# Optimization experiments

Hardware: AMD Instinct MI355X
Metric: run time of the kernel (lower is better)

Reference implementation:

```python
import jax, jax.numpy as jnp
import numpy as np

D = 512       # d_model
H = 8         # n_heads
L = 6         # n_blocks
DFF = 2048    # d_ffn
IN_DIM = 4096
OUT_DIM = 1000
B = 8
S = 512
DK = D // H
EPS = 1e-5
NEG = -1e9    # masked_fill value from source (-1000000000.0)

# sinusoidal positional encoding table (matches Positional_Encoding)
_pos = np.arange(5000)[:, None].astype(np.float64)
_div = np.exp(np.arange(0, D, 2) * (-np.log(10000.0) / D))
_pe = np.zeros((5000, D), np.float32)
_pe[:, 0::2] = np.sin(_pos * _div)
_pe[:, 1::2] = np.cos(_pos * _div)
PE = jnp.asarray(_pe)


def _ln(x, g, b):
    m = jnp.mean(x, -1, keepdims=True)
    v = jnp.var(x, -1, keepdims=True)
    return (x - m) * jax.lax.rsqrt(v + EPS) * g + b


def _attn(q, k, v, causal):
    # q:[B,Sq,D], k/v:[B,Sk,D] -> multi-head attention with source's quirky mask
    b, sq, _ = q.shape
    sk = k.shape[1]
    q = q.reshape(b, sq, H, DK).transpose(0, 2, 1, 3)
    k = k.reshape(b, sk, H, DK).transpose(0, 2, 1, 3)
    v = v.reshape(b, sk, H, DK).transpose(0, 2, 1, 3)
    s = jnp.einsum('bhqd,bhkd->bhqk', q, k) / jnp.sqrt(jnp.asarray(DK, q.dtype))
    mask = s != 0.0  # faithful: source masks positions where score == padding (0)
    if causal:
        mask = mask & jnp.tril(jnp.ones((sq, sk), bool))
    s = jnp.where(mask, s, NEG)
    p = jax.nn.softmax(s, axis=-1)
    o = jnp.einsum('bhqk,bhkd->bhqd', p, v)
    return o.transpose(0, 2, 1, 3).reshape(b, sq, D)


def _ffn(x, w1, b1, w2, b2):
    return jax.nn.relu(x @ w1 + b1) @ w2 + b2


def setup_inputs() -> dict:
    key = jax.random.key(0)
    ks = iter(jax.random.split(key, 40))

    def w(shape, s=0.02):
        return jax.random.normal(next(ks), shape, jnp.float32) * s

    inp = {}
    inp['x'] = jax.random.randint(next(ks), (B, S), 0, IN_DIM)
    inp['target'] = jax.random.randint(next(ks), (B,), 0, OUT_DIM)
    inp['in_emb'] = w((IN_DIM, D), 1.0)
    inp['out_emb'] = w((OUT_DIM, D), 1.0)
    # encoder params (stacked over layers)
    inp['enc_qkv_w'] = w((L, 3, D, D))
    inp['enc_qkv_b'] = w((L, 3, D))
    inp['enc_ln1_g'] = jnp.ones((L, D), jnp.float32)
    inp['enc_ln1_b'] = jnp.zeros((L, D), jnp.float32)
    inp['enc_ffn1_w'] = w((L, D, DFF))
    inp['enc_ffn1_b'] = w((L, DFF))
    inp['enc_ffn2_w'] = w((L, DFF, D))
    inp['enc_ffn2_b'] = w((L, D))
    inp['enc_ln2_g'] = jnp.ones((L, D), jnp.float32)
    inp['enc_ln2_b'] = jnp.zeros((L, D), jnp.float32)
    # decoder params
    inp['dec_qkv1_w'] = w((L, 3, D, D))
    inp['dec_qkv1_b'] = w((L, 3, D))
    inp['dec_ln1_g'] = jnp.ones((L, D), jnp.float32)
    inp['dec_ln1_b'] = jnp.zeros((L, D), jnp.float32)
    inp['dec_qkv2_w'] = w((L, 3, D, D))
    inp['dec_qkv2_b'] = w((L, 3, D))
    inp['dec_ln2_g'] = jnp.ones((L, D), jnp.float32)
    inp['dec_ln2_b'] = jnp.zeros((L, D), jnp.float32)
    inp['dec_ffn1_w'] = w((L, D, DFF))
    inp['dec_ffn1_b'] = w((L, DFF))
    inp['dec_ffn2_w'] = w((L, DFF, D))
    inp['dec_ffn2_b'] = w((L, D))
    inp['dec_ln3_g'] = jnp.ones((L, D), jnp.float32)
    inp['dec_ln3_b'] = jnp.zeros((L, D), jnp.float32)
    inp['out_w'] = w((D, OUT_DIM))
    inp['out_b'] = w((OUT_DIM,))
    return inp


def reference(x, target, in_emb, out_emb,
              enc_qkv_w, enc_qkv_b, enc_ln1_g, enc_ln1_b,
              enc_ffn1_w, enc_ffn1_b, enc_ffn2_w, enc_ffn2_b,
              enc_ln2_g, enc_ln2_b,
              dec_qkv1_w, dec_qkv1_b, dec_ln1_g, dec_ln1_b,
              dec_qkv2_w, dec_qkv2_b, dec_ln2_g, dec_ln2_b,
              dec_ffn1_w, dec_ffn1_b, dec_ffn2_w, dec_ffn2_b,
              dec_ln3_g, dec_ln3_b, out_w, out_b):
    scale = jnp.sqrt(jnp.float32(D))
    # encoder: embed tokens + positional encoding (dropout is identity at eval)
    e = in_emb[x] * scale + PE[None, :S]
    for i in range(L):
        q = e @ enc_qkv_w[i, 0] + enc_qkv_b[i, 0]
        k = e @ enc_qkv_w[i, 1] + enc_qkv_b[i, 1]
        v = e @ enc_qkv_w[i, 2] + enc_qkv_b[i, 2]
        e = _ln(_attn(q, k, v, False) + e, enc_ln1_g[i], enc_ln1_b[i])
        e = _ln(e + _ffn(e, enc_ffn1_w[i], enc_ffn1_b[i], enc_ffn2_w[i], enc_ffn2_b[i]),
                enc_ln2_g[i], enc_ln2_b[i])
    # decoder: target.unsqueeze(1) -> seq len 1
    d = out_emb[target][:, None, :] * scale + PE[None, :1]
    for i in range(L):
        q = d @ dec_qkv1_w[i, 0] + dec_qkv1_b[i, 0]
        k = d @ dec_qkv1_w[i, 1] + dec_qkv1_b[i, 1]
        v = d @ dec_qkv1_w[i, 2] + dec_qkv1_b[i, 2]
        d = _ln(_attn(q, k, v, True) + d, dec_ln1_g[i], dec_ln1_b[i])
        q = d @ dec_qkv2_w[i, 0] + dec_qkv2_b[i, 0]
        k = e @ dec_qkv2_w[i, 1] + dec_qkv2_b[i, 1]
        v = e @ dec_qkv2_w[i, 2] + dec_qkv2_b[i, 2]
        d = _ln(_attn(q, k, v, False) + d, dec_ln2_g[i], dec_ln2_b[i])
        d = _ln(d + _ffn(d, dec_ffn1_w[i], dec_ffn1_b[i], dec_ffn2_w[i], dec_ffn2_b[i]),
                dec_ln3_g[i], dec_ln3_b[i])
    return d @ out_w + out_b  # [B, 1, OUT_DIM] logits (source never applies its softmax)
```

## Files before the change

### kernel.cpp

```cpp
#include <hip/hip_runtime.h>
#include <hip/hip_bf16.h>

#define DM 512
#define NH 8
#define DK 64
#define SEQ 512
#define NB 8
#define NL 6
#define DFF 2048
#define OUTD 1000
#define EMB_SCALE 22.627416997969522f
#define PE_C (-0.017988946039015984f)

typedef __bf16 bf16x8 __attribute__((ext_vector_type(8)));
typedef __bf16 bf16x4 __attribute__((ext_vector_type(4)));
typedef float f32x4 __attribute__((ext_vector_type(4)));

__device__ __forceinline__ void load16_lds(const __bf16* g, __bf16* l) {
  __builtin_amdgcn_global_load_lds(
      (const __attribute__((address_space(1))) void*)g,
      (__attribute__((address_space(3))) void*)l, 16, 0, 0);
}

__device__ __forceinline__ float dot8(bf16x8 w, const float* a) {
  float s = 0.f;
#pragma unroll
  for (int j = 0; j < 8; ++j) s += (float)w[j] * a[j];
  return s;
}

__global__ __launch_bounds__(256) void pe_kernel(float* __restrict__ pe) {
  int s = blockIdx.x;
  int d2 = threadIdx.x;
  float div = expf((float)(2 * d2) * PE_C);
  float arg = (float)s * div;
  pe[(size_t)s * DM + 2 * d2] = sinf(arg);
  pe[(size_t)s * DM + 2 * d2 + 1] = cosf(arg);
}

__global__ __launch_bounds__(256) void embed_enc(const int* __restrict__ x,
                                                 const float* __restrict__ emb,
                                                 const float* __restrict__ pe,
                                                 float* __restrict__ e,
                                                 __bf16* __restrict__ eb) {
  int idx = blockIdx.x * 256 + threadIdx.x;
  int d = idx & (DM - 1);
  int bs = idx >> 9;
  int s = bs & (SEQ - 1);
  int tok = x[bs];
  float v = emb[(size_t)tok * DM + d] * EMB_SCALE + pe[(size_t)s * DM + d];
  e[idx] = v;
  eb[idx] = (__bf16)v;
}

__global__ __launch_bounds__(256) void embed_dec(const int* __restrict__ t,
                                                 const float* __restrict__ emb,
                                                 float* __restrict__ dd) {
  int idx = blockIdx.x * 256 + threadIdx.x;
  int d = idx & (DM - 1);
  int b = idx >> 9;
  float pe = (d & 1) ? 1.0f : 0.0f;
  dd[idx] = emb[(size_t)t[b] * DM + d] * EMB_SCALE + pe;
}

__global__ __launch_bounds__(256) void transpose_w(const float* __restrict__ W,
                                                   __bf16* __restrict__ WT,
                                                   int K, int N) {
  __shared__ float t[32][33];
  size_t off = (size_t)blockIdx.z * K * N;
  W += off; WT += off;
  int k0 = blockIdx.y * 32, n0 = blockIdx.x * 32;
  int tx = threadIdx.x & 7, ty = threadIdx.x >> 3;
  float4 v = *(const float4*)&W[(size_t)(k0 + ty) * N + n0 + tx * 4];
  t[ty][tx * 4 + 0] = v.x; t[ty][tx * 4 + 1] = v.y;
  t[ty][tx * 4 + 2] = v.z; t[ty][tx * 4 + 3] = v.w;
  __syncthreads();
  bf16x4 o;
  o[0] = (__bf16)t[tx * 4 + 0][ty];
  o[1] = (__bf16)t[tx * 4 + 1][ty];
  o[2] = (__bf16)t[tx * 4 + 2][ty];
  o[3] = (__bf16)t[tx * 4 + 3][ty];
  *(bf16x4*)&WT[(size_t)(n0 + ty) * K + k0 + tx * 4] = o;
}

__global__ __launch_bounds__(256) void transpose_ow(const float* __restrict__ W,
                                                    __bf16* __restrict__ WT) {
  __shared__ float t[32][33];
  int n0 = blockIdx.x * 32, k0 = blockIdx.y * 32;
  int tid = threadIdx.x;
  for (int i = tid; i < 1024; i += 256) {
    int kk = i >> 5, nn = i & 31;
    t[kk][nn] = (n0 + nn < OUTD) ? W[(size_t)(k0 + kk) * OUTD + n0 + nn] : 0.f;
  }
  __syncthreads();
  for (int i = tid; i < 1024; i += 256) {
    int nn = i >> 5, kk = i & 31;
    if (n0 + nn < OUTD)
      WT[(size_t)(n0 + nn) * DM + k0 + kk] = (__bf16)t[kk][nn];
  }
}

template <int BN, bool RELU, bool WF32, bool WBF16, bool TRV, bool KVM>
__global__ __launch_bounds__(512) void mfma_gemm(
    const __bf16* __restrict__ A, const __bf16* __restrict__ BT,
    const float* __restrict__ bias, float* __restrict__ C,
    __bf16* __restrict__ Cb, __bf16* __restrict__ Vt, int M, int N, int K,
    long btStride, long bStride, long cStride) {
  int gx = gridDim.x, gy = gridDim.y;
  int lin = blockIdx.x + gx * (blockIdx.y + gy * blockIdx.z);
  int xcd = lin & 7, li = lin >> 3;
  int yc = gy >> 3;
  int bx = li % gx;
  int t2 = li / gx;
  int by = xcd * yc + (t2 % yc);
  int z = t2 / yc;

  if (KVM) {
    long idx = (long)(z >> 1) * 3 + 1 + (z & 1);
    BT += idx * btStride;
    bias += idx * bStride;
  } else {
    BT += (size_t)z * btStride;
    bias += (size_t)z * bStride;
  }
  if (WF32) C += (size_t)z * cStride;
  if (WBF16) Cb += (size_t)z * cStride;

  constexpr int NI = BN / 32;
  __shared__ __bf16 As[2][128 * 64];
  __shared__ __bf16 Bs[2][BN * 64];

  int tid = threadIdx.x;
  int wave = tid >> 6, lane = tid & 63;
  int wm = wave >> 1, wn = wave & 1;
  int quad = lane >> 4, l16 = lane & 15;
  int rlane = lane >> 3, c8 = lane & 7;
  int m0 = by * 128, n0 = bx * BN;
  int gcol = ((c8 ^ rlane) * 8);

  f32x4 acc[2][NI];
#pragma unroll
  for (int i = 0; i < 2; ++i)
#pragma unroll
    for (int j = 0; j < NI; ++j) acc[i][j] = (f32x4){0.f, 0.f, 0.f, 0.f};

  auto stage = [&](int buf, int k0) {
#pragma unroll
    for (int j = 0; j < 2; ++j) {
      int rb = j * 64 + wave * 8;
      load16_lds(&A[(size_t)(m0 + rb + rlane) * K + k0 + gcol],
                 &As[buf][rb * 64]);
    }
#pragma unroll
    for (int j = 0; j < BN / 64; ++j) {
      int rb = j * 64 + wave * 8;
      load16_lds(&BT[(size_t)(n0 + rb + rlane) * K + k0 + gcol],
                 &Bs[buf][rb * 64]);
    }
  };

  const int NT = K >> 6;
  stage(0, 0);
  __syncthreads();
  for (int t = 0; t < NT; ++t) {
    int cur = t & 1;
    if (t + 1 < NT) stage(cur ^ 1, (t + 1) << 6);
#pragma unroll
    for (int kk = 0; kk < 64; kk += 32) {
      bf16x8 af[2], bfr[NI];
#pragma unroll
      for (int i = 0; i < 2; ++i) {
        int row = wm * 32 + i * 16 + l16;
        af[i] = *(const bf16x8*)&As[cur][row * 64 + ((((kk >> 3) + quad) ^ (row & 7)) * 8)];
      }
#pragma unroll
      for (int i = 0; i < NI; ++i) {
        int row = wn * (BN / 2) + i * 16 + l16;
        bfr[i] = *(const bf16x8*)&Bs[cur][row * 64 + ((((kk >> 3) + quad) ^ (row & 7)) * 8)];
      }
#pragma unroll
      for (int mi = 0; mi < 2; ++mi)
#pragma unroll
        for (int ni = 0; ni < NI; ++ni)
          acc[mi][ni] = __builtin_amdgcn_mfma_f32_16x16x32_bf16(
              af[mi], bfr[ni], acc[mi][ni], 0, 0, 0);
    }
    __syncthreads();
  }

#pragma unroll
  for (int ni = 0; ni < NI; ++ni) {
    int col = n0 + wn * (BN / 2) + ni * 16 + l16;
    float bv = bias[col];
    if (TRV && z == 2) {
      int b = m0 >> 9;
#pragma unroll
      for (int mi = 0; mi < 2; ++mi) {
        int srow = (m0 & 511) + wm * 32 + mi * 16 + quad * 4;
        bf16x4 pk;
#pragma unroll
        for (int r = 0; r < 4; ++r) pk[r] = (__bf16)(acc[mi][ni][r] + bv);
        *(bf16x4*)&Vt[((size_t)(b * 512 + col)) * 512 + srow] = pk;
      }
    } else {
#pragma unroll
      for (int mi = 0; mi < 2; ++mi) {
#pragma unroll
        for (int r = 0; r < 4; ++r) {
          int row = m0 + wm * 32 + mi * 16 + quad * 4 + r;
          float v = acc[mi][ni][r] + bv;
          if (RELU) v = fmaxf(v, 0.f);
          if (WF32) C[(size_t)row * N + col] = v;
          if (WBF16) Cb[(size_t)row * N + col] = (__bf16)v;
        }
      }
    }
  }
}

#define SCP 520
__global__ __launch_bounds__(256) void attn_mfma(const __bf16* __restrict__ QKV,
                                                 const __bf16* __restrict__ Vt,
                                                 float* __restrict__ O) {
  __shared__ __bf16 Sc[16 * SCP];
  __shared__ __bf16 Tt[2][64 * 64];

  const long ACTL = (long)NB * SEQ * DM;
  int tid = threadIdx.x;
  int wave = tid >> 6, lane = tid & 63;
  int quad = lane >> 4, l16 = lane & 15;
  int rlane = lane >> 3, c8 = lane & 7;
  int lin = blockIdx.x + gridDim.x * blockIdx.y;
  int xcd = lin & 7, li = lin >> 3;
  int yc = gridDim.y >> 3;
  int q0 = (li % gridDim.x) * 16;
  int bh = xcd * yc + li / gridDim.x;
  int b = bh >> 3, h = bh & 7;
  const __bf16* Q = QKV;
  const __bf16* Kp = QKV + ACTL;
  size_t baseQ = ((size_t)b * SEQ + q0) * DM + h * DK;
  size_t baseK = ((size_t)b * SEQ) * DM + h * DK;
  const __bf16* VtB = Vt + ((size_t)(b * 512 + h * 64)) * 512;
  int gcol = (c8 ^ rlane) * 8;

  bf16x8 af0 = *(const bf16x8*)&Q[baseQ + (size_t)l16 * DM + quad * 8];
  bf16x8 af1 = *(const bf16x8*)&Q[baseQ + (size_t)l16 * DM + 32 + quad * 8];

  auto stageK = [&](int buf, int kt) {
#pragma unroll
    for (int j = 0; j < 2; ++j) {
      int row = j * 32 + wave * 8 + rlane;
      load16_lds(&Kp[baseK + (size_t)(kt * 64 + row) * DM + gcol],
                 &Tt[buf][(j * 32 + wave * 8) * 64]);
    }
  };
  auto stageV = [&](int buf, int kt) {
#pragma unroll
    for (int j = 0; j < 2; ++j) {
      int row = j * 32 + wave * 8 + rlane;
      load16_lds(&VtB[(size_t)row * 512 + kt * 64 + gcol],
                 &Tt[buf][(j * 32 + wave * 8) * 64]);
    }
  };

  stageK(0, 0);
  __syncthreads();
  for (int kt = 0; kt < 8; ++kt) {
    int cur = kt & 1;
    if (kt < 7) stageK(cur ^ 1, kt + 1);
    f32x4 acc = (f32x4){0.f, 0.f, 0.f, 0.f};
    int krow = wave * 16 + l16, sw = krow & 7;
    bf16x8 b0 = *(const bf16x8*)&Tt[cur][krow * 64 + ((quad ^ sw) * 8)];
    bf16x8 b1 = *(const bf16x8*)&Tt[cur][krow * 64 + (((4 + quad) ^ sw) * 8)];
    acc = __builtin_amdgcn_mfma_f32_16x16x32_bf16(af0, b0, acc, 0, 0, 0);
    acc = __builtin_amdgcn_mfma_f32_16x16x32_bf16(af1, b1, acc, 0, 0, 0);
#pragma unroll
    for (int r = 0; r < 4; ++r)
      Sc[(quad * 4 + r) * SCP + kt * 64 + wave * 16 + l16] =
          (__bf16)(acc[r] * 0.125f);
    __syncthreads();
  }

  stageV(0, 0);

#pragma unroll
  for (int rr = 0; rr < 4; ++rr) {
    int r = wave * 4 + rr;
    float v[8];
    float mx = -1e30f;
#pragma unroll
    for (int j = 0; j < 8; ++j) {
      v[j] = (float)Sc[r * SCP + j * 64 + lane];
      mx = fmaxf(mx, v[j]);
    }
    for (int o = 32; o > 0; o >>= 1) mx = fmaxf(mx, __shfl_xor(mx, o));
    float sum = 0.f;
#pragma unroll
    for (int j = 0; j < 8; ++j) { v[j] = __expf(v[j] - mx); sum += v[j]; }
    for (int o = 32; o > 0; o >>= 1) sum += __shfl_xor(sum, o);
    float inv = 1.f / sum;
#pragma unroll
    for (int j = 0; j < 8; ++j)
      Sc[r * SCP + j * 64 + lane] = (__bf16)(v[j] * inv);
  }
  __syncthreads();

  f32x4 oacc = (f32x4){0.f, 0.f, 0.f, 0.f};
  for (int kt = 0; kt < 8; ++kt) {
    int cur = kt & 1;
    if (kt < 7) stageV(cur ^ 1, kt + 1);
    int drow = wave * 16 + l16, sw = drow & 7;
#pragma unroll
    for (int kk = 0; kk < 64; kk += 32) {
      bf16x8 pa = *(const bf16x8*)&Sc[l16 * SCP + kt * 64 + kk + quad * 8];
      bf16x8 vb = *(const bf16x8*)&Tt[cur][drow * 64 + ((((kk >> 3) + quad) ^ sw) * 8)];
      oacc = __builtin_amdgcn_mfma_f32_16x16x32_bf16(pa, vb, oacc, 0, 0, 0);
    }
    __syncthreads();
  }
#pragma unroll
  for (int r = 0; r < 4; ++r)
    O[((size_t)b * SEQ + q0 + quad * 4 + r) * DM + h * DK + wave * 16 + l16] =
        oacc[r];
}

template <bool WB>
__global__ __launch_bounds__(256) void add_ln(
    const float* __restrict__ x, const float* __restrict__ res,
    const float* __restrict__ cbias,
    const float* __restrict__ g, const float* __restrict__ beta,
    float* __restrict__ y, __bf16* __restrict__ yb) {
  int row = blockIdx.x;
  int tid = threadIdx.x;
  const float* xr = x + (size_t)row * DM;
  const float* rr = res + (size_t)row * DM;
  float b0 = cbias ? cbias[tid] : 0.f;
  float b1 = cbias ? cbias[tid + 256] : 0.f;
  float v0 = xr[tid] + b0 + rr[tid];
  float v1 = xr[tid + 256] + b1 + rr[tid + 256];
  float s = v0 + v1, sq = v0 * v0 + v1 * v1;
  for (int o = 32; o > 0; o >>= 1) {
    s += __shfl_xor(s, o);
    sq += __shfl_xor(sq, o);
  }
  __shared__ float ps[4], pq[4];
  int wv = tid >> 6;
  if ((tid & 63) == 0) { ps[wv] = s; pq[wv] = sq; }
  __syncthreads();
  s = ps[0] + ps[1] + ps[2] + ps[3];
  sq = pq[0] + pq[1] + pq[2] + pq[3];
  float mean = s * (1.f / DM);
  float var = sq * (1.f / DM) - mean * mean;
  float rstd = rsqrtf(var + 1e-5f);
  float o0 = (v0 - mean) * rstd * g[tid] + beta[tid];
  float o1 = (v1 - mean) * rstd * g[tid + 256] + beta[tid + 256];
  y[(size_t)row * DM + tid] = o0;
  y[(size_t)row * DM + tid + 256] = o1;
  if (WB) {
    yb[(size_t)row * DM + tid] = (__bf16)o0;
    yb[(size_t)row * DM + tid + 256] = (__bf16)o1;
  }
}


__global__ __launch_bounds__(256) void dec_vln(
    float* __restrict__ dd, const __bf16* __restrict__ WvT,
    const float* __restrict__ bv, const float* __restrict__ g,
    const float* __restrict__ beta) {
  __shared__ float arow[DM];
  int r = blockIdx.x, tid = threadIdx.x;
  arow[tid] = dd[(size_t)r * DM + tid];
  arow[tid + 256] = dd[(size_t)r * DM + tid + 256];
  __syncthreads();
  float out[2];
#pragma unroll
  for (int cc = 0; cc < 2; ++cc) {
    int c = tid + cc * 256;
    const __bf16* w = &WvT[(size_t)c * DM];
    float acc = 0.f;
#pragma unroll 4
    for (int k = 0; k < DM; k += 8) acc += dot8(*(const bf16x8*)&w[k], &arow[k]);
    out[cc] = arow[c] + acc + bv[c];
  }
  float s = out[0] + out[1], sq = out[0] * out[0] + out[1] * out[1];
  for (int o = 32; o > 0; o >>= 1) { s += __shfl_xor(s, o); sq += __shfl_xor(sq, o); }
  __shared__ float ps[4], pq[4];
  int wv = tid >> 6;
  if ((tid & 63) == 0) { ps[wv] = s; pq[wv] = sq; }
  __syncthreads();
  s = ps[0] + ps[1] + ps[2] + ps[3];
  sq = pq[0] + pq[1] + pq[2] + pq[3];
  float mean = s * (1.f / DM);
  float rstd = rsqrtf(sq * (1.f / DM) - mean * mean + 1e-5f);
  dd[(size_t)r * DM + tid] = (out[0] - mean) * rstd * g[tid] + beta[tid];
  dd[(size_t)r * DM + tid + 256] = (out[1] - mean) * rstd * g[tid + 256] + beta[tid + 256];
}

__global__ __launch_bounds__(256) void dec_qattn(
    const float* __restrict__ dd, const __bf16* __restrict__ WqT,
    const float* __restrict__ qb, const __bf16* __restrict__ Kb,
    const __bf16* __restrict__ Vb, float* __restrict__ da) {
  __shared__ float arow[DM];
  __shared__ float red[4][64];
  __shared__ float q[64];
  __shared__ float sc[SEQ];
  __shared__ float wred[4];

  int bh = blockIdx.x, b = bh >> 3, h = bh & 7;
  int tid = threadIdx.x, lane = tid & 63, wave = tid >> 6;
  arow[tid] = dd[(size_t)b * DM + tid];
  arow[tid + 256] = dd[(size_t)b * DM + tid + 256];
  __syncthreads();

  {
    int c = tid & 63, s = tid >> 6;
    const __bf16* w = &WqT[(size_t)(h * 64 + c) * DM + s * 128];
    float acc = 0.f;
#pragma unroll
    for (int k = 0; k < 128; k += 8) acc += dot8(*(const bf16x8*)&w[k], &arow[s * 128 + k]);
    red[s][c] = acc;
  }
  __syncthreads();
  if (tid < 64) q[tid] = red[0][tid] + red[1][tid] + red[2][tid] + red[3][tid] + qb[h * 64 + tid];
  __syncthreads();

  for (int key = tid; key < SEQ; key += 256) {
    const __bf16* kp = &Kb[((size_t)b * SEQ + key) * DM + h * 64];
    float acc = 0.f;
#pragma unroll
    for (int k = 0; k < 64; k += 8) acc += dot8(*(const bf16x8*)&kp[k], &q[k]);
    sc[key] = acc * 0.125f;
  }
  __syncthreads();
  float m = -1e30f;
  for (int j = tid; j < SEQ; j += 256) m = fmaxf(m, sc[j]);
  for (int o = 32; o > 0; o >>= 1) m = fmaxf(m, __shfl_xor(m, o));
  if (lane == 0) wred[wave] = m;
  __syncthreads();
  m = fmaxf(fmaxf(wred[0], wred[1]), fmaxf(wred[2], wred[3]));
  float sum = 0.f;
  for (int j = tid; j < SEQ; j += 256) {
    float p = __expf(sc[j] - m);
    sc[j] = p;
    sum += p;
  }
  for (int o = 32; o > 0; o >>= 1) sum += __shfl_xor(sum, o);
  __syncthreads();
  if (lane == 0) wred[wave] = sum;
  __syncthreads();
  float inv = 1.f / (wred[0] + wred[1] + wred[2] + wred[3]);

  {
    int d = tid & 63, s = tid >> 6;
    float acc = 0.f;
    const __bf16* vp = &Vb[((size_t)b * SEQ + s * 128) * DM + h * 64 + d];
#pragma unroll 8
    for (int k = 0; k < 128; ++k) acc += sc[s * 128 + k] * (float)vp[(size_t)k * DM];
    red[s][d] = acc;
  }
  __syncthreads();
  if (tid < 64)
    da[(size_t)b * DM + h * 64 + tid] =
        (red[0][tid] + red[1][tid] + red[2][tid] + red[3][tid]) * inv;
}

__global__ __launch_bounds__(256) void dec_ffn1(
    const float* __restrict__ dd, const __bf16* __restrict__ W1T,
    const float* __restrict__ b1, float* __restrict__ h) {
  __shared__ float a[8][DM];
  int tid = threadIdx.x, lane = tid & 63, wave = tid >> 6;
  for (int i = tid; i < 8 * DM; i += 256) a[i >> 9][i & 511] = dd[i];
  __syncthreads();
  int col = blockIdx.x * 4 + wave;
  bf16x8 w = *(const bf16x8*)&W1T[(size_t)col * DM + lane * 8];
  float acc[8];
#pragma unroll
  for (int r = 0; r < 8; ++r) acc[r] = dot8(w, &a[r][lane * 8]);
#pragma unroll
  for (int r = 0; r < 8; ++r)
    for (int o = 32; o > 0; o >>= 1) acc[r] += __shfl_xor(acc[r], o);
  if (lane == 0) {
    float bb = b1[col];
#pragma unroll
    for (int r = 0; r < 8; ++r) h[(size_t)r * DFF + col] = fmaxf(acc[r] + bb, 0.f);
  }
}

__global__ __launch_bounds__(256) void dec_ffn2(
    const float* __restrict__ h, const __bf16* __restrict__ W2T,
    const float* __restrict__ b2, float* __restrict__ df) {
  __shared__ float red[4][8];
  int tid = threadIdx.x, lane = tid & 63, wave = tid >> 6;
  int c = wave >> 1, half = wave & 1;
  int col = blockIdx.x * 2 + c;
  int k0 = half * 1024 + lane * 8;
  bf16x8 w0 = *(const bf16x8*)&W2T[(size_t)col * DFF + k0];
  bf16x8 w1 = *(const bf16x8*)&W2T[(size_t)col * DFF + k0 + 512];
  float acc[8];
#pragma unroll
  for (int r = 0; r < 8; ++r) {
    float4 h0a = *(const float4*)&h[(size_t)r * DFF + k0];
    float4 h0b = *(const float4*)&h[(size_t)r * DFF + k0 + 4];
    float4 h1a = *(const float4*)&h[(size_t)r * DFF + k0 + 512];
    float4 h1b = *(const float4*)&h[(size_t)r * DFF + k0 + 516];
    float hh0[8] = {h0a.x, h0a.y, h0a.z, h0a.w, h0b.x, h0b.y, h0b.z, h0b.w};
    float hh1[8] = {h1a.x, h1a.y, h1a.z, h1a.w, h1b.x, h1b.y, h1b.z, h1b.w};
    acc[r] = dot8(w0, hh0) + dot8(w1, hh1);
  }
#pragma unroll
  for (int r = 0; r < 8; ++r)
    for (int o = 32; o > 0; o >>= 1) acc[r] += __shfl_xor(acc[r], o);
  if (lane == 0) {
#pragma unroll
    for (int r = 0; r < 8; ++r) red[wave][r] = acc[r];
  }
  __syncthreads();
  if (tid < 16) {
    int cc = tid >> 3, r = tid & 7;
    int ocol = blockIdx.x * 2 + cc;
    df[(size_t)r * DM + ocol] =
        red[cc * 2][r] + red[cc * 2 + 1][r] + b2[ocol];
  }
}

__global__ __launch_bounds__(256) void dec_out(
    const float* __restrict__ dd, const __bf16* __restrict__ WoT,
    const float* __restrict__ ob, float* __restrict__ out) {
  __shared__ float a[8][DM];
  int tid = threadIdx.x, lane = tid & 63, wave = tid >> 6;
  for (int i = tid; i < 8 * DM; i += 256) a[i >> 9][i & 511] = dd[i];
  __syncthreads();
  int col = blockIdx.x * 4 + wave;
  bf16x8 w = *(const bf16x8*)&WoT[(size_t)col * DM + lane * 8];
  float acc[8];
#pragma unroll
  for (int r = 0; r < 8; ++r) acc[r] = dot8(w, &a[r][lane * 8]);
#pragma unroll
  for (int r = 0; r < 8; ++r)
    for (int o = 32; o > 0; o >>= 1) acc[r] += __shfl_xor(acc[r], o);
  if (lane == 0) {
    float bb = ob[col];
#pragma unroll
    for (int r = 0; r < 8; ++r) out[(size_t)r * OUTD + col] = acc[r] + bb;
  }
}

extern "C" void kernel_launch(void* const* d_in, const int* in_sizes, int n_in,
                              void* d_out, int out_size, void* d_ws, size_t ws_size,
                              hipStream_t stream) {
  const int* x = (const int*)d_in[0];
  const int* target = (const int*)d_in[1];
  const float* in_emb = (const float*)d_in[2];
  const float* out_emb = (const float*)d_in[3];
  const float* enc_qkv_w = (const float*)d_in[4];
  const float* enc_qkv_b = (const float*)d_in[5];
  const float* enc_ln1_g = (const float*)d_in[6];
  const float* enc_ln1_b = (const float*)d_in[7];
  const float* enc_ffn1_w = (const float*)d_in[8];
  const float* enc_ffn1_b = (const float*)d_in[9];
  const float* enc_ffn2_w = (const float*)d_in[10];
  const float* enc_ffn2_b = (const float*)d_in[11];
  const float* enc_ln2_g = (const float*)d_in[12];
  const float* enc_ln2_b = (const float*)d_in[13];
  const float* dec_qkv1_w = (const float*)d_in[14];
  const float* dec_qkv1_b = (const float*)d_in[15];
  const float* dec_ln1_g = (const float*)d_in[16];
  const float* dec_ln1_b = (const float*)d_in[17];
  const float* dec_qkv2_w = (const float*)d_in[18];
  const float* dec_qkv2_b = (const float*)d_in[19];
  const float* dec_ln2_g = (const float*)d_in[20];
  const float* dec_ln2_b = (const float*)d_in[21];
  const float* dec_ffn1_w = (const float*)d_in[22];
  const float* dec_ffn1_b = (const float*)d_in[23];
  const float* dec_ffn2_w = (const float*)d_in[24];
  const float* dec_ffn2_b = (const float*)d_in[25];
  const float* dec_ln3_g = (const float*)d_in[26];
  const float* dec_ln3_b = (const float*)d_in[27];
  const float* out_w = (const float*)d_in[28];
  const float* out_b = (const float*)d_in[29];

  const long ACTL = (long)NB * SEQ * DM;
  const int M = NB * SEQ;
  const long WQS = (long)DM * DM;
  const long WFS = (long)DM * DFF;

  char* p = (char*)d_ws;
  float* e = (float*)p;            p += ACTL * 4;
  float* tb = (float*)p;           p += ACTL * 4;
  float* pe = (float*)p;           p += (long)SEQ * DM * 4;
  float* dd = (float*)p;           p += NB * DM * 4;
  float* da = (float*)p;           p += NB * DM * 4;
  float* dh = (float*)p;           p += NB * DFF * 4;
  float* df = (float*)p;           p += NB * DM * 4;
  p = (char*)(((uintptr_t)p + 255) & ~(uintptr_t)255);
  __bf16* eb = (__bf16*)p;         p += ACTL * 2;
  __bf16* qkvb = (__bf16*)p;       p += 3 * ACTL * 2;
  __bf16* hbb = (__bf16*)p;        p += (long)M * DFF * 2;
  __bf16* kvb = (__bf16*)p;        p += 12L * ACTL * 2;
  __bf16* wtq = (__bf16*)p;        p += 18L * WQS * 2;
  __bf16* wtf1 = (__bf16*)p;       p += 6L * WFS * 2;
  __bf16* wtf2 = (__bf16*)p;       p += 6L * WFS * 2;
  __bf16* wtd = (__bf16*)p;        p += 18L * WQS * 2;
  __bf16* wtd1 = (__bf16*)p;       p += 18L * WQS * 2;
  __bf16* wf1t = (__bf16*)p;       p += 6L * WFS * 2;
  __bf16* wf2t = (__bf16*)p;       p += 6L * WFS * 2;
  __bf16* wot = (__bf16*)p;        p += (long)OUTD * DM * 2;

  __bf16* vtb = qkvb + 2 * ACTL;

  pe_kernel<<<SEQ, 256, 0, stream>>>(pe);
  transpose_w<<<dim3(16, 16, 18), 256, 0, stream>>>(enc_qkv_w, wtq, DM, DM);
  transpose_w<<<dim3(64, 16, 6), 256, 0, stream>>>(enc_ffn1_w, wtf1, DM, DFF);
  transpose_w<<<dim3(16, 64, 6), 256, 0, stream>>>(enc_ffn2_w, wtf2, DFF, DM);
  transpose_w<<<dim3(16, 16, 18), 256, 0, stream>>>(dec_qkv2_w, wtd, DM, DM);
  transpose_w<<<dim3(16, 16, 18), 256, 0, stream>>>(dec_qkv1_w, wtd1, DM, DM);
  transpose_w<<<dim3(64, 16, 6), 256, 0, stream>>>(dec_ffn1_w, wf1t, DM, DFF);
  transpose_w<<<dim3(16, 64, 6), 256, 0, stream>>>(dec_ffn2_w, wf2t, DFF, DM);
  transpose_ow<<<dim3(32, 16), 256, 0, stream>>>(out_w, wot);

  embed_enc<<<(M * DM) / 256, 256, 0, stream>>>(x, in_emb, pe, e, eb);
  for (int i = 0; i < NL; ++i) {
    mfma_gemm<128, false, false, true, true, false><<<dim3(4, 32, 3), 512, 0, stream>>>(
        eb, wtq + (size_t)i * 3 * WQS, enc_qkv_b + (size_t)i * 3 * DM,
        nullptr, qkvb, vtb, M, DM, DM, WQS, DM, ACTL);
    attn_mfma<<<dim3(SEQ / 16, NB * NH), 256, 0, stream>>>(qkvb, vtb, tb);
    add_ln<true><<<M, 256, 0, stream>>>(tb, e, nullptr, enc_ln1_g + i * DM,
                                        enc_ln1_b + i * DM, e, eb);
    mfma_gemm<128, true, false, true, false, false><<<dim3(16, 32, 1), 512, 0, stream>>>(
        eb, wtf1 + (size_t)i * WFS, enc_ffn1_b + (size_t)i * DFF,
        nullptr, hbb, nullptr, M, DFF, DM, 0, 0, 0);
    mfma_gemm<64, false, true, false, false, false><<<dim3(8, 32, 1), 512, 0, stream>>>(
        hbb, wtf2 + (size_t)i * WFS, enc_ffn2_b + (size_t)i * DM,
        tb, nullptr, nullptr, M, DM, DFF, 0, 0, 0);
    add_ln<true><<<M, 256, 0, stream>>>(tb, e, nullptr, enc_ln2_g + i * DM,
                                        enc_ln2_b + i * DM, e, eb);
  }

  mfma_gemm<128, false, false, true, false, true><<<dim3(4, 32, 12), 512, 0, stream>>>(
      eb, wtd, dec_qkv2_b, nullptr, kvb, nullptr, M, DM, DM, WQS, DM, ACTL);

  embed_dec<<<(NB * DM) / 256, 256, 0, stream>>>(target, out_emb, dd);
  for (int i = 0; i < NL; ++i) {
    dec_vln<<<8, 256, 0, stream>>>(
        dd, wtd1 + ((size_t)i * 3 + 2) * WQS, dec_qkv1_b + ((size_t)i * 3 + 2) * DM,
        dec_ln1_g + i * DM, dec_ln1_b + i * DM);
    dec_qattn<<<64, 256, 0, stream>>>(
        dd, wtd + (size_t)i * 3 * WQS, dec_qkv2_b + (size_t)i * 3 * DM,
        kvb + (size_t)i * 2 * ACTL, kvb + ((size_t)i * 2 + 1) * ACTL, da);
    add_ln<false><<<NB, 256, 0, stream>>>(
        da, dd, nullptr, dec_ln2_g + i * DM, dec_ln2_b + i * DM, dd, nullptr);
    dec_ffn1<<<DFF / 4, 256, 0, stream>>>(
        dd, wf1t + (size_t)i * WFS, dec_ffn1_b + (size_t)i * DFF, dh);
    dec_ffn2<<<DM / 2, 256, 0, stream>>>(
        dh, wf2t + (size_t)i * WFS, dec_ffn2_b + (size_t)i * DM, df);
    add_ln<false><<<NB, 256, 0, stream>>>(
        df, dd, nullptr, dec_ln3_g + i * DM, dec_ln3_b + i * DM, dd, nullptr);
  }

  dec_out<<<OUTD / 4, 256, 0, stream>>>(dd, wot, out_b, (float*)d_out);
}
```

Before: 1.157 ms.

## Retile GEMMs to 4-wave blocks and split-K FFN2 with reduction fused into layernorm

The MFMA GEMM drops from 8 waves to 4 per block, with each wave now covering 64 rows (4x16 M fragments) instead of 32, and BN shrinks from 128 to 64 so the grids grow. The encoder FFN2 GEMM (K=2048) is split into two K halves writing separate fp32 partials, with the second partial placed in the kvb scratch buffer. add_ln gains an optional second input that sums the partials. The aim is better occupancy and CU coverage for the small-N and long-K GEMMs, at the cost of an extra fp32 partial write and read and more register pressure per wave. It reuses kvb as scratch before the decoder KV GEMM overwrites it.

```diff
diff --git a/kernel.cpp b/kernel.cpp
--- a/kernel.cpp
+++ b/kernel.cpp
@@ -100,8 +100,8 @@
   }
 }
 
-template <int BN, bool RELU, bool WF32, bool WBF16, bool TRV, bool KVM>
-__global__ __launch_bounds__(512) void mfma_gemm(
+template <int BN, int SK, bool RELU, bool WF32, bool WBF16, bool TRV, bool KVM>
+__global__ __launch_bounds__(256) void mfma_gemm(
     const __bf16* __restrict__ A, const __bf16* __restrict__ BT,
     const float* __restrict__ bias, float* __restrict__ C,
     __bf16* __restrict__ Cb, __bf16* __restrict__ Vt, int M, int N, int K,
@@ -115,13 +115,15 @@
   int by = xcd * yc + (t2 % yc);
   int z = t2 / yc;
 
-  if (KVM) {
-    long idx = (long)(z >> 1) * 3 + 1 + (z & 1);
-    BT += idx * btStride;
-    bias += idx * bStride;
-  } else {
-    BT += (size_t)z * btStride;
-    bias += (size_t)z * bStride;
+  if (SK == 1) {
+    if (KVM) {
+      long idx = (long)(z >> 1) * 3 + 1 + (z & 1);
+      BT += idx * btStride;
+      bias += idx * bStride;
+    } else {
+      BT += (size_t)z * btStride;
+      bias += (size_t)z * bStride;
+    }
   }
   if (WF32) C += (size_t)z * cStride;
   if (WBF16) Cb += (size_t)z * cStride;
@@ -138,39 +140,41 @@
   int m0 = by * 128, n0 = bx * BN;
   int gcol = ((c8 ^ rlane) * 8);
 
-  f32x4 acc[2][NI];
-#pragma unroll
-  for (int i = 0; i < 2; ++i)
+  f32x4 acc[4][NI];
+#pragma unroll
+  for (int i = 0; i < 4; ++i)
 #pragma unroll
     for (int j = 0; j < NI; ++j) acc[i][j] = (f32x4){0.f, 0.f, 0.f, 0.f};
 
   auto stage = [&](int buf, int k0) {
 #pragma unroll
-    for (int j = 0; j < 2; ++j) {
-      int rb = j * 64 + wave * 8;
+    for (int j = 0; j < 4; ++j) {
+      int rb = j * 32 + wave * 8;
       load16_lds(&A[(size_t)(m0 + rb + rlane) * K + k0 + gcol],
                  &As[buf][rb * 64]);
     }
 #pragma unroll
-    for (int j = 0; j < BN / 64; ++j) {
-      int rb = j * 64 + wave * 8;
+    for (int j = 0; j < BN / 32; ++j) {
+      int rb = j * 32 + wave * 8;
       load16_lds(&BT[(size_t)(n0 + rb + rlane) * K + k0 + gcol],
                  &Bs[buf][rb * 64]);
     }
   };
 
-  const int NT = K >> 6;
-  stage(0, 0);
+  int kLen = (SK > 1) ? (K / SK) : K;
+  int kBeg = (SK > 1) ? z * kLen : 0;
+  const int NT = kLen >> 6;
+  stage(0, kBeg);
   __syncthreads();
   for (int t = 0; t < NT; ++t) {
     int cur = t & 1;
-    if (t + 1 < NT) stage(cur ^ 1, (t + 1) << 6);
+    if (t + 1 < NT) stage(cur ^ 1, kBeg + ((t + 1) << 6));
 #pragma unroll
     for (int kk = 0; kk < 64; kk += 32) {
-      bf16x8 af[2], bfr[NI];
-#pragma unroll
-      for (int i = 0; i < 2; ++i) {
-        int row = wm * 32 + i * 16 + l16;
+      bf16x8 af[4], bfr[NI];
+#pragma unroll
+      for (int i = 0; i < 4; ++i) {
+        int row = wm * 64 + i * 16 + l16;
         af[i] = *(const bf16x8*)&As[cur][row * 64 + ((((kk >> 3) + quad) ^ (row & 7)) * 8)];
       }
 #pragma unroll
@@ -179,7 +183,7 @@
         bfr[i] = *(const bf16x8*)&Bs[cur][row * 64 + ((((kk >> 3) + quad) ^ (row & 7)) * 8)];
       }
 #pragma unroll
-      for (int mi = 0; mi < 2; ++mi)
+      for (int mi = 0; mi < 4; ++mi)
 #pragma unroll
         for (int ni = 0; ni < NI; ++ni)
           acc[mi][ni] = __builtin_amdgcn_mfma_f32_16x16x32_bf16(
@@ -191,12 +195,12 @@
 #pragma unroll
   for (int ni = 0; ni < NI; ++ni) {
     int col = n0 + wn * (BN / 2) + ni * 16 + l16;
-    float bv = bias[col];
+    float bv = (SK == 1 || z == 0) ? bias[col] : 0.f;
     if (TRV && z == 2) {
       int b = m0 >> 9;
 #pragma unroll
-      for (int mi = 0; mi < 2; ++mi) {
-        int srow = (m0 & 511) + wm * 32 + mi * 16 + quad * 4;
+      for (int mi = 0; mi < 4; ++mi) {
+        int srow = (m0 & 511) + wm * 64 + mi * 16 + quad * 4;
         bf16x4 pk;
 #pragma unroll
         for (int r = 0; r < 4; ++r) pk[r] = (__bf16)(acc[mi][ni][r] + bv);
@@ -204,10 +208,10 @@
       }
     } else {
 #pragma unroll
-      for (int mi = 0; mi < 2; ++mi) {
+      for (int mi = 0; mi < 4; ++mi) {
 #pragma unroll
         for (int r = 0; r < 4; ++r) {
-          int row = m0 + wm * 32 + mi * 16 + quad * 4 + r;
+          int row = m0 + wm * 64 + mi * 16 + quad * 4 + r;
           float v = acc[mi][ni][r] + bv;
           if (RELU) v = fmaxf(v, 0.f);
           if (WF32) C[(size_t)row * N + col] = v;
@@ -326,8 +330,8 @@
 
 template <bool WB>
 __global__ __launch_bounds__(256) void add_ln(
-    const float* __restrict__ x, const float* __restrict__ res,
-    const float* __restrict__ cbias,
+    const float* __restrict__ x, const float* __restrict__ x2,
+    const float* __restrict__ res, const float* __restrict__ cbias,
     const float* __restrict__ g, const float* __restrict__ beta,
     float* __restrict__ y, __bf16* __restrict__ yb) {
   int row = blockIdx.x;
@@ -338,6 +342,11 @@
   float b1 = cbias ? cbias[tid + 256] : 0.f;
   float v0 = xr[tid] + b0 + rr[tid];
   float v1 = xr[tid + 256] + b1 + rr[tid + 256];
+  if (x2) {
+    const float* x2r = x2 + (size_t)row * DM;
+    v0 += x2r[tid];
+    v1 += x2r[tid + 256];
+  }
   float s = v0 + v1, sq = v0 * v0 + v1 * v1;
   for (int o = 32; o > 0; o >>= 1) {
     s += __shfl_xor(s, o);
@@ -607,6 +616,8 @@
   __bf16* wot = (__bf16*)p;        p += (long)OUTD * DM * 2;
 
   __bf16* vtb = qkvb + 2 * ACTL;
+  float* tb2 = (float*)kvb;
+  long tb2Off = (long)(tb2 - tb);
 
   pe_kernel<<<SEQ, 256, 0, stream>>>(pe);
   transpose_w<<<dim3(16, 16, 18), 256, 0, stream>>>(enc_qkv_w, wtq, DM, DM);
@@ -620,23 +631,25 @@
 
   embed_enc<<<(M * DM) / 256, 256, 0, stream>>>(x, in_emb, pe, e, eb);
   for (int i = 0; i < NL; ++i) {
-    mfma_gemm<128, false, false, true, true, false><<<dim3(4, 32, 3), 512, 0, stream>>>(
+    mfma_gemm<64, 1, false, false, true, true, false><<<dim3(8, 32, 3), 256, 0, stream>>>(
         eb, wtq + (size_t)i * 3 * WQS, enc_qkv_b + (size_t)i * 3 * DM,
         nullptr, qkvb, vtb, M, DM, DM, WQS, DM, ACTL);
     attn_mfma<<<dim3(SEQ / 16, NB * NH), 256, 0, stream>>>(qkvb, vtb, tb);
-    add_ln<true><<<M, 256, 0, stream>>>(tb, e, nullptr, enc_ln1_g + i * DM,
-                                        enc_ln1_b + i * DM, e, eb);
-    mfma_gemm<128, true, false, true, false, false><<<dim3(16, 32, 1), 512, 0, stream>>>(
+    add_ln<true><<<M, 256, 0, stream>>>(tb, nullptr, e, nullptr,
+                                        enc_ln1_g + i * DM, enc_ln1_b + i * DM,
+                                        e, eb);
+    mfma_gemm<64, 1, true, false, true, false, false><<<dim3(32, 32, 1), 256, 0, stream>>>(
         eb, wtf1 + (size_t)i * WFS, enc_ffn1_b + (size_t)i * DFF,
         nullptr, hbb, nullptr, M, DFF, DM, 0, 0, 0);
-    mfma_gemm<64, false, true, false, false, false><<<dim3(8, 32, 1), 512, 0, stream>>>(
+    mfma_gemm<64, 2, false, true, false, false, false><<<dim3(8, 32, 2), 256, 0, stream>>>(
         hbb, wtf2 + (size_t)i * WFS, enc_ffn2_b + (size_t)i * DM,
-        tb, nullptr, nullptr, M, DM, DFF, 0, 0, 0);
-    add_ln<true><<<M, 256, 0, stream>>>(tb, e, nullptr, enc_ln2_g + i * DM,
-                                        enc_ln2_b + i * DM, e, eb);
-  }
-
-  mfma_gemm<128, false, false, true, false, true><<<dim3(4, 32, 12), 512, 0, stream>>>(
+        tb, nullptr, nullptr, M, DM, DFF, 0, 0, tb2Off);
+    add_ln<true><<<M, 256, 0, stream>>>(tb, tb2, e, nullptr,
+                                        enc_ln2_g + i * DM, enc_ln2_b + i * DM,
+                                        e, eb);
+  }
+
+  mfma_gemm<64, 1, false, false, true, false, true><<<dim3(8, 32, 12), 256, 0, stream>>>(
       eb, wtd, dec_qkv2_b, nullptr, kvb, nullptr, M, DM, DM, WQS, DM, ACTL);
 
   embed_dec<<<(NB * DM) / 256, 256, 0, stream>>>(target, out_emb, dd);
@@ -648,13 +661,15 @@
         dd, wtd + (size_t)i * 3 * WQS, dec_qkv2_b + (size_t)i * 3 * DM,
         kvb + (size_t)i * 2 * ACTL, kvb + ((size_t)i * 2 + 1) * ACTL, da);
     add_ln<false><<<NB, 256, 0, stream>>>(
-        da, dd, nullptr, dec_ln2_g + i * DM, dec_ln2_b + i * DM, dd, nullptr);
+        da, nullptr, dd, nullptr, dec_ln2_g + i * DM, dec_ln2_b + i * DM,
+        dd, nullptr);
     dec_ffn1<<<DFF / 4, 256, 0, stream>>>(
         dd, wf1t + (size_t)i * WFS, dec_ffn1_b + (size_t)i * DFF, dh);
     dec_ffn2<<<DM / 2, 256, 0, stream>>>(
         dh, wf2t + (size_t)i * WFS, dec_ffn2_b + (size_t)i * DM, df);
     add_ln<false><<<NB, 256, 0, stream>>>(
-        df, dd, nullptr, dec_ln3_g + i * DM, dec_ln3_b + i * DM, dd, nullptr);
+        df, nullptr, dd, nullptr, dec_ln3_g + i * DM, dec_ln3_b + i * DM,
+        dd, nullptr);
   }
 
   dec_out<<<OUTD / 4, 256, 0, stream>>>(dd, wot, out_b, (float*)d_out);
```

After: 1.149 ms. About the same (-0.7%).
